# Kernel optimization log

Measured on AMD Instinct MI355X. Metric: run time of the kernel, lower is better.

Reference implementation:

```python
import jax, jax.numpy as jnp
import numpy as np
from jax import lax

EPS = 1e-5

def setup_inputs() -> dict:
    key = jax.random.key(0)
    k1, k2, k3, k4, k5 = jax.random.split(key, 5)
    N, Cin, L = 64, 64, 8192
    Cout, K = 128, 7
    return {
        "I": jax.random.normal(k1, (N, Cin, L), dtype=jnp.float32),
        "gamma": jax.random.uniform(k2, (Cin,), dtype=jnp.float32, minval=0.5, maxval=1.5),
        "beta": jax.random.normal(k3, (Cin,), dtype=jnp.float32) * 0.1,
        "W": jax.random.normal(k4, (Cout, Cin, K), dtype=jnp.float32) * 0.05,
        "alpha": jax.random.uniform(k5, (Cout, 1), dtype=jnp.float32, minval=0.01, maxval=0.2),
    }

def reference(I, gamma, beta, W, alpha):
    # BatchNorm1d (training mode: batch stats over N and L, biased variance)
    mean = jnp.mean(I, axis=(0, 2), keepdims=True)           # [1,C,1]
    var = jnp.mean(jnp.square(I - mean), axis=(0, 2), keepdims=True)
    x = (I - mean) * lax.rsqrt(var + EPS)
    x = x * gamma[None, :, None] + beta[None, :, None]
    # Binarize: sign with 0 -> +1
    xb = jnp.where(x >= 0, jnp.float32(1.0), jnp.float32(-1.0))
    # Conv1d (no bias), stride 1, pad 3; NCH x OIH -> NCH
    y = lax.conv_general_dilated(
        xb, W, window_strides=(1,), padding=[(3, 3)],
        dimension_numbers=("NCH", "OIH", "NCH"))
    # per-output-channel alpha scale: alpha [O,1] -> broadcast [1,O,1]
    y = y * alpha[None, :, :]
    # MaxPool1d(kernel=2, stride=2)
    y = lax.reduce_window(y, -jnp.inf, lax.max,
                          window_dimensions=(1, 1, 2),
                          window_strides=(1, 1, 2),
                          padding="VALID")
    return y  # [64, 128, 4096]
```

## Files before the change

### kernel.cpp

```cpp
#include <hip/hip_runtime.h>
#include <hip/hip_bf16.h>


#define N_S   64
#define C_IN  64
#define L_IN  8192
#define C_OUT 128
#define KW    7
#define L_OUT 4096
#define KDIM  448
#define XROWS 8200

typedef float  fx4   __attribute__((ext_vector_type(4)));
typedef short  s16x8 __attribute__((ext_vector_type(8)));

typedef __bf16 bfx8  __attribute__((ext_vector_type(8)));
template <typename V> struct OtherFrag          { typedef bfx8  type; };
template <>           struct OtherFrag<bfx8>    { typedef s16x8 type; };

template <typename V>
static __device__ inline auto mfma_sel(V a, V b, fx4 c, int)
    -> decltype(__builtin_amdgcn_mfma_f32_16x16x32_bf16(a, b, c, 0, 0, 0)) {
  return __builtin_amdgcn_mfma_f32_16x16x32_bf16(a, b, c, 0, 0, 0);
}
template <typename V>
static __device__ inline fx4 mfma_sel(V a, V b, fx4 c, long) {
  typedef typename OtherFrag<V>::type O;
  return __builtin_amdgcn_mfma_f32_16x16x32_bf16(
      __builtin_bit_cast(O, a), __builtin_bit_cast(O, b), c, 0, 0, 0);
}
static __device__ inline fx4 mfma_bf16(s16x8 a, s16x8 b, fx4 c) {
  return mfma_sel(a, b, c, 0);
}

static __device__ inline unsigned short bin_sign(float I, float m, float s,
                                                 float g, float b) {
  float x = __fadd_rn(__fmul_rn(__fmul_rn(__fsub_rn(I, m), s), g), b);
  return (x >= 0.0f) ? (unsigned short)0x3F80 : (unsigned short)0xBF80;
}

__global__ __launch_bounds__(256)
void bnstats_kernel(const float* __restrict__ x_in, double* __restrict__ partials) {
  const int c = blockIdx.x, g = blockIdx.y, tid = threadIdx.x;
  double sum = 0.0, sq = 0.0;
  for (int ns = 0; ns < 2; ++ns) {
    const float4* b4 =
        (const float4*)(x_in + ((size_t)((g * 2 + ns) * C_IN + c) << 13));
#pragma unroll
    for (int j = 0; j < 8; ++j) {
      float4 v = b4[j * 256 + tid];
      double dx = v.x, dy = v.y, dz = v.z, dw = v.w;
      sum += (dx + dy) + (dz + dw);
      sq  += (dx * dx + dy * dy) + (dz * dz + dw * dw);
    }
  }
  for (int off = 32; off > 0; off >>= 1) {
    sum += __shfl_down(sum, off);
    sq  += __shfl_down(sq,  off);
  }
  __shared__ double sd[8];
  const int wv = tid >> 6;
  if ((tid & 63) == 0) { sd[wv * 2] = sum; sd[wv * 2 + 1] = sq; }
  __syncthreads();
  if (tid == 0) {
    double S = sd[0] + sd[2] + sd[4] + sd[6];
    double Q = sd[1] + sd[3] + sd[5] + sd[7];
    partials[(c * 32 + g) * 2]     = S;
    partials[(c * 32 + g) * 2 + 1] = Q;
  }
}

__global__ void bnreduce_kernel(const double* __restrict__ partials,
                                const float* __restrict__ gamma,
                                const float* __restrict__ beta,
                                float4* __restrict__ bnparams) {
  const int c = threadIdx.x;
  if (c < C_IN) {
    double S = 0.0, Q = 0.0;
    for (int g = 0; g < 32; ++g) {
      S += partials[(c * 32 + g) * 2];
      Q += partials[(c * 32 + g) * 2 + 1];
    }
    const double NL = (double)N_S * (double)L_IN;
    double mean_d = S / NL;
    float  mean_f = (float)mean_d;
    double var_d = Q / NL - 2.0 * (double)mean_f * mean_d +
                   (double)mean_f * (double)mean_f;
    float var_f = (float)var_d;
    float vpe   = __fadd_rn(var_f, 1e-5f);
    float s_f   = (float)(1.0 / sqrt((double)vpe));
    bnparams[c] = make_float4(mean_f, s_f, gamma[c], beta[c]);
  }
}

__global__ __launch_bounds__(256)
void wrepack_kernel(const float* __restrict__ W, unsigned short* __restrict__ Wr) {
  const int f = blockIdx.x * 256 + threadIdx.x;
  if (f < C_OUT * KDIM) {
    const int o = f / KDIM, rem = f - o * KDIM;
    const int c = rem / KW, k = rem - c * KW;
    unsigned int u = __builtin_bit_cast(unsigned int, W[f]);
    u += 0x7FFFu + ((u >> 16) & 1u);
    Wr[o * KDIM + k * C_IN + c] = (unsigned short)(u >> 16);
  }
}

__global__ __launch_bounds__(256)
void bintrans2_kernel(const float* __restrict__ x_in,
                      const float4* __restrict__ bnparams,
                      unsigned short* __restrict__ xbt) {
  const int chunk = blockIdx.x, n = blockIdx.y, tid = threadIdx.x;
  const int lbase = chunk * 256;
  const int lane = tid & 63, w = tid >> 6;
  __shared__ __align__(16) char ldsT[256 * 128];

  const int fidx = (lbase >> 2) + lane;
#pragma unroll
  for (int cc = 0; cc < 4; ++cc) {
    const int c0 = w * 16 + cc * 4;
    const float4 bp0 = bnparams[c0 + 0];
    const float4 bp1 = bnparams[c0 + 1];
    const float4 bp2 = bnparams[c0 + 2];
    const float4 bp3 = bnparams[c0 + 3];
    const float4 f0 = ((const float4*)(x_in + ((size_t)(n * C_IN + c0 + 0) << 13)))[fidx];
    const float4 f1 = ((const float4*)(x_in + ((size_t)(n * C_IN + c0 + 1) << 13)))[fidx];
    const float4 f2 = ((const float4*)(x_in + ((size_t)(n * C_IN + c0 + 2) << 13)))[fidx];
    const float4 f3 = ((const float4*)(x_in + ((size_t)(n * C_IN + c0 + 3) << 13)))[fidx];
    const float e0[4] = {f0.x, f0.y, f0.z, f0.w};
    const float e1[4] = {f1.x, f1.y, f1.z, f1.w};
    const float e2[4] = {f2.x, f2.y, f2.z, f2.w};
    const float e3[4] = {f3.x, f3.y, f3.z, f3.w};
#pragma unroll
    for (int d = 0; d < 4; ++d) {
      ushort4 v;
      v.x = bin_sign(e0[d], bp0.x, bp0.y, bp0.z, bp0.w);
      v.y = bin_sign(e1[d], bp1.x, bp1.y, bp1.z, bp1.w);
      v.z = bin_sign(e2[d], bp2.x, bp2.y, bp2.z, bp2.w);
      v.w = bin_sign(e3[d], bp3.x, bp3.y, bp3.z, bp3.w);
      const int l   = 4 * lane + d;
      const int key = ((l & 7) ^ ((l >> 3) & 7)) << 4;
      *(ushort4*)(ldsT + l * 128 + ((c0 * 2) ^ key)) = v;
    }
  }
  __syncthreads();

  char* gout = (char*)xbt + (size_t)n * XROWS * 128 + (size_t)(lbase + 3) * 128;
#pragma unroll
  for (int i = 0; i < 8; ++i) {
    const int idx  = i * 256 + tid;
    const int row  = idx >> 3, slot = idx & 7;
    const int key  = ((row & 7) ^ ((row >> 3) & 7)) << 4;
    *(int4*)(gout + ((size_t)idx << 4)) =
        *(const int4*)(ldsT + row * 128 + ((slot << 4) ^ key));
  }
  int4 z4; z4.x = z4.y = z4.z = z4.w = 0;
  if (chunk == 0 && tid < 24)
    *(int4*)((char*)xbt + (size_t)n * XROWS * 128 + tid * 16) = z4;
  if (chunk == 31 && tid < 40)
    *(int4*)((char*)xbt + (size_t)n * XROWS * 128 + 8195ull * 128 + tid * 16) = z4;
}

__global__ __launch_bounds__(256)
void bconv3_kernel(const unsigned short* __restrict__ xbt,
                   const unsigned short* __restrict__ Wr,
                   const float* __restrict__ alpha,
                   float* __restrict__ out) {
  const int n     = blockIdx.z;
  const int obase = blockIdx.y * 64;
  const int lbase = blockIdx.x * 256;
  const int tid  = threadIdx.x;
  const int lane = tid & 63, w = tid >> 6;
  const int n16 = lane & 15, quad = lane >> 4;
  const int lW = w * 64;

  __shared__ __align__(16) char ldsB[264 * 128];

  {
    const char* gbase =
        (const char*)(xbt + (size_t)n * XROWS * C_IN) + (size_t)lbase * 128;
    const int r_in = lane >> 3;
    const int colb = (lane & 7) << 4;
    for (int i = w; i < 33; i += 4) {
      const int row = i * 8 + r_in;
      const char* src = gbase + row * 128 + (colb ^ ((row & 7) << 4));
      __builtin_amdgcn_global_load_lds((const unsigned int*)src,
                                       (unsigned int*)(ldsB + i * 1024),
                                       16, 0, 0);
    }
  }
  __syncthreads();

  fx4 acc[4][4];
#pragma unroll
  for (int ob = 0; ob < 4; ++ob)
#pragma unroll
    for (int lb = 0; lb < 4; ++lb)
      acc[ob][lb] = (fx4){0.f, 0.f, 0.f, 0.f};

  const unsigned short* arow = Wr + (obase + n16) * KDIM + quad * 8;

#pragma unroll
  for (int ks = 0; ks < 14; ++ks) {
    const int k  = ks >> 1;
    const int cb = ((ks & 1) << 6) | (quad << 4);
    s16x8 afr[4];
#pragma unroll
    for (int ob = 0; ob < 4; ++ob)
      afr[ob] = *(const s16x8*)(arow + ob * 16 * KDIM + ks * 32);
    s16x8 bfr[4];
#pragma unroll
    for (int lb = 0; lb < 4; ++lb) {
      const int row = lW + lb * 16 + n16 + k;
      bfr[lb] = *(const s16x8*)(ldsB + row * 128 + (cb ^ ((row & 7) << 4)));
    }
#pragma unroll
    for (int ob = 0; ob < 4; ++ob)
#pragma unroll
      for (int lb = 0; lb < 4; ++lb)
        acc[ob][lb] = mfma_bf16(afr[ob], bfr[lb], acc[ob][lb]);
  }

  float al[16];
#pragma unroll
  for (int ob = 0; ob < 4; ++ob)
#pragma unroll
    for (int r = 0; r < 4; ++r)
      al[ob * 4 + r] = alpha[obase + ob * 16 + quad * 4 + r];

  const size_t outbase = (size_t)n * C_OUT * L_OUT;
#pragma unroll
  for (int ob = 0; ob < 4; ++ob) {
#pragma unroll
    for (int lb = 0; lb < 4; ++lb) {
      const int l_local = lW + lb * 16 + n16;
#pragma unroll
      for (int r = 0; r < 4; ++r) {
        const int o = obase + ob * 16 + quad * 4 + r;
        float v  = acc[ob][lb][r];
        float pv = __shfl_xor(v, 1);
        float mx = fmaxf(v, pv);
        if ((n16 & 1) == 0) {
          out[outbase + (size_t)o * L_OUT + ((lbase + l_local) >> 1)] =
              mx * al[ob * 4 + r];
        }
      }
    }
  }
}

#define LT    64
#define PROWS 70
#define RS    72
__global__ __launch_bounds__(256)
void bconv_fused_kernel(const float* __restrict__ x_in,
                        const float4* __restrict__ bnparams,
                        const float* __restrict__ alpha,
                        const unsigned short* __restrict__ Wr,
                        float* __restrict__ out) {
  const int tile = blockIdx.x, n = blockIdx.y;
  const int l0 = tile * LT, tid = threadIdx.x;
  __shared__ __align__(16) unsigned short lds_xb[PROWS * RS];
  {
    const int c = tid >> 2, sub = tid & 3;
    const float4 bp = bnparams[c];
    const float* xc = x_in + ((size_t)(n * C_IN + c) << 13);
#pragma unroll
    for (int i = 0; i < 18; ++i) {
      const int p = sub * 18 + i;
      if (p < PROWS) {
        const int l = l0 + p - 3;
        unsigned short v = 0;
        if (l >= 0 && l < L_IN) v = bin_sign(xc[l], bp.x, bp.y, bp.z, bp.w);
        lds_xb[p * RS + c] = v;
      }
    }
  }
  __syncthreads();
  const int lane = tid & 63, w = tid >> 6;
  const int n16 = lane & 15, quad = lane >> 4;
  const int obase = (w & 1) * 64, lwave = (w >> 1) * 32;
  fx4 acc[4][2];
#pragma unroll
  for (int ob = 0; ob < 4; ++ob)
#pragma unroll
    for (int lb = 0; lb < 2; ++lb) acc[ob][lb] = (fx4){0.f, 0.f, 0.f, 0.f};
  const unsigned short* arow = Wr + (obase + n16) * KDIM + quad * 8;
#pragma unroll
  for (int ks = 0; ks < 14; ++ks) {
    const int k = ks >> 1, c0 = (ks & 1) * 32;
    s16x8 afr[4];
#pragma unroll
    for (int ob = 0; ob < 4; ++ob)
      afr[ob] = *(const s16x8*)(arow + ob * 16 * KDIM + ks * 32);
    s16x8 bfr[2];
#pragma unroll
    for (int lb = 0; lb < 2; ++lb) {
      const int p = lwave + lb * 16 + n16 + k;
      bfr[lb] = *(const s16x8*)(&lds_xb[p * RS + c0 + quad * 8]);
    }
#pragma unroll
    for (int ob = 0; ob < 4; ++ob)
#pragma unroll
      for (int lb = 0; lb < 2; ++lb)
        acc[ob][lb] = mfma_bf16(afr[ob], bfr[lb], acc[ob][lb]);
  }
  const size_t outbase = (size_t)n * C_OUT * L_OUT;
#pragma unroll
  for (int ob = 0; ob < 4; ++ob)
#pragma unroll
    for (int lb = 0; lb < 2; ++lb) {
      const int l_local = lwave + lb * 16 + n16;
#pragma unroll
      for (int r = 0; r < 4; ++r) {
        const int o = obase + ob * 16 + quad * 4 + r;
        float v = acc[ob][lb][r];
        float pv = __shfl_xor(v, 1);
        float mx = fmaxf(v, pv);
        if ((n16 & 1) == 0)
          out[outbase + (size_t)o * L_OUT + ((l0 + l_local) >> 1)] = mx * alpha[o];
      }
    }
}

extern "C" void kernel_launch(void* const* d_in, const int* in_sizes, int n_in,
                              void* d_out, int out_size, void* d_ws, size_t ws_size,
                              hipStream_t stream) {
  const float* x_in  = (const float*)d_in[0];
  const float* gamma = (const float*)d_in[1];
  const float* beta  = (const float*)d_in[2];
  const float* W     = (const float*)d_in[3];
  const float* alpha = (const float*)d_in[4];
  float* out = (float*)d_out;

  double*         partials = (double*)d_ws;
  float4*         bnparams = (float4*)((char*)d_ws + 32768);
  unsigned short* Wr       = (unsigned short*)((char*)d_ws + 36864);
  unsigned short* xbt      = (unsigned short*)((char*)d_ws + 262144);
  const size_t xbt_bytes   = (size_t)N_S * XROWS * C_IN * 2;

  bnstats_kernel<<<dim3(64, 32), 256, 0, stream>>>(x_in, partials);
  wrepack_kernel<<<(C_OUT * KDIM + 255) / 256, 256, 0, stream>>>(W, Wr);
  bnreduce_kernel<<<1, 64, 0, stream>>>(partials, gamma, beta, bnparams);

  if (ws_size >= 262144 + xbt_bytes) {
    bintrans2_kernel<<<dim3(32, 64), 256, 0, stream>>>(x_in, bnparams, xbt);
    bconv3_kernel<<<dim3(32, 2, 64), 256, 0, stream>>>(xbt, Wr, alpha, out);
  } else {
    bconv_fused_kernel<<<dim3(128, 64), 256, 0, stream>>>(x_in, bnparams,
                                                          alpha, Wr, out);
  }
}
```

Measured before the change: 423.5 us.

## Make bconv persistent with register-resident weights and double-buffered LDS staging

Replaces the one-tile-per-block conv with a kernel where each block loops over 16 L-tiles of 128. The full weight fragment set for 64 output channels stays in registers for the whole loop, and the next input tile is staged into LDS through a double buffer while the current one computes. Waves are split 2x2 over output channels and L. This cuts repeated weight loads from global memory and hides load latency. In exchange it uses a very large register footprint (occupancy bound of 1 block), and the grid shrinks to 256 blocks, which may underfill the GPU.

New measurement: 385.7 us. -8.9%, faster.

```diff
diff --git a/kernel.cpp b/kernel.cpp
--- a/kernel.cpp
+++ b/kernel.cpp
@@ -160,88 +160,107 @@
     *(int4*)((char*)xbt + (size_t)n * XROWS * 128 + 8195ull * 128 + tid * 16) = z4;
 }
 
-__global__ __launch_bounds__(256)
-void bconv3_kernel(const unsigned short* __restrict__ xbt,
+__global__ __launch_bounds__(256, 1)
+void bconv4_kernel(const unsigned short* __restrict__ xbt,
                    const unsigned short* __restrict__ Wr,
                    const float* __restrict__ alpha,
                    float* __restrict__ out) {
-  const int n     = blockIdx.z;
-  const int obase = blockIdx.y * 64;
-  const int lbase = blockIdx.x * 256;
+  const int n  = blockIdx.y;
+  const int lq = blockIdx.x;
   const int tid  = threadIdx.x;
   const int lane = tid & 63, w = tid >> 6;
   const int n16 = lane & 15, quad = lane >> 4;
-  const int lW = w * 64;
-
-  __shared__ __align__(16) char ldsB[264 * 128];
-
+  const int obase = (w & 1) * 64;
+  const int lW    = (w >> 1) * 64;
+
+  __shared__ __align__(16) char ldsB[2][136 * 128];
+
+  s16x8 areg[14][4];
   {
-    const char* gbase =
-        (const char*)(xbt + (size_t)n * XROWS * C_IN) + (size_t)lbase * 128;
-    const int r_in = lane >> 3;
-    const int colb = (lane & 7) << 4;
-    for (int i = w; i < 33; i += 4) {
+    const unsigned short* arow = Wr + (obase + n16) * KDIM + quad * 8;
+#pragma unroll
+    for (int ks = 0; ks < 14; ++ks)
+#pragma unroll
+      for (int ob = 0; ob < 4; ++ob)
+        areg[ks][ob] = *(const s16x8*)(arow + ob * 16 * KDIM + ks * 32);
+  }
+  float al[16];
+#pragma unroll
+  for (int ob = 0; ob < 4; ++ob)
+#pragma unroll
+    for (int r = 0; r < 4; ++r)
+      al[ob * 4 + r] = alpha[obase + ob * 16 + quad * 4 + r];
+
+  const char* gB = (const char*)(xbt + (size_t)n * XROWS * C_IN);
+  const int r_in = lane >> 3;
+  const int colb = (lane & 7) << 4;
+  const int lq0  = lq * 2048;
+
+  auto stage = [&](int t, int buf) {
+    const char* gbase = gB + (size_t)(lq0 + t * 128) * 128;
+    for (int i = w; i < 17; i += 4) {
       const int row = i * 8 + r_in;
       const char* src = gbase + row * 128 + (colb ^ ((row & 7) << 4));
       __builtin_amdgcn_global_load_lds((const unsigned int*)src,
-                                       (unsigned int*)(ldsB + i * 1024),
+                                       (unsigned int*)(&ldsB[buf][i * 1024]),
                                        16, 0, 0);
     }
-  }
+  };
+
+  stage(0, 0);
+  asm volatile("s_waitcnt vmcnt(0)");
   __syncthreads();
 
-  fx4 acc[4][4];
-#pragma unroll
-  for (int ob = 0; ob < 4; ++ob)
-#pragma unroll
-    for (int lb = 0; lb < 4; ++lb)
-      acc[ob][lb] = (fx4){0.f, 0.f, 0.f, 0.f};
-
-  const unsigned short* arow = Wr + (obase + n16) * KDIM + quad * 8;
-
-#pragma unroll
-  for (int ks = 0; ks < 14; ++ks) {
-    const int k  = ks >> 1;
-    const int cb = ((ks & 1) << 6) | (quad << 4);
-    s16x8 afr[4];
+  const size_t outbase = (size_t)n * C_OUT * L_OUT;
+  int buf = 0;
+  for (int t = 0; t < 16; ++t) {
+    if (t < 15) stage(t + 1, buf ^ 1);
+
+    fx4 acc[4][4];
 #pragma unroll
     for (int ob = 0; ob < 4; ++ob)
-      afr[ob] = *(const s16x8*)(arow + ob * 16 * KDIM + ks * 32);
-    s16x8 bfr[4];
-#pragma unroll
-    for (int lb = 0; lb < 4; ++lb) {
-      const int row = lW + lb * 16 + n16 + k;
-      bfr[lb] = *(const s16x8*)(ldsB + row * 128 + (cb ^ ((row & 7) << 4)));
-    }
-#pragma unroll
-    for (int ob = 0; ob < 4; ++ob)
 #pragma unroll
       for (int lb = 0; lb < 4; ++lb)
-        acc[ob][lb] = mfma_bf16(afr[ob], bfr[lb], acc[ob][lb]);
-  }
-
-  float al[16];
-#pragma unroll
-  for (int ob = 0; ob < 4; ++ob)
-#pragma unroll
-    for (int r = 0; r < 4; ++r)
-      al[ob * 4 + r] = alpha[obase + ob * 16 + quad * 4 + r];
-
-  const size_t outbase = (size_t)n * C_OUT * L_OUT;
-#pragma unroll
-  for (int ob = 0; ob < 4; ++ob) {
-#pragma unroll
-    for (int lb = 0; lb < 4; ++lb) {
-      const int l_local = lW + lb * 16 + n16;
-#pragma unroll
-      for (int r = 0; r < 4; ++r) {
-        const int o = obase + ob * 16 + quad * 4 + r;
-        float v  = acc[ob][lb][r];
-        float pv = __shfl_xor(v, 1);
-        float mx = fmaxf(v, pv);
-        if ((n16 & 1) == 0) {
-          out[outbase + (size_t)o * L_OUT + ((lbase + l_local) >> 1)] =
-              mx * al[ob * 4 + r];
+        acc[ob][lb] = (fx4){0.f, 0.f, 0.f, 0.f};
+
+    const char* Bb = ldsB[buf];
+#pragma unroll
+    for (int ks = 0; ks < 14; ++ks) {
+      const int k  = ks >> 1;
+      const int cb = ((ks & 1) << 6) | (quad << 4);
+      s16x8 bfr[4];
+#pragma unroll
+      for (int lb = 0; lb < 4; ++lb) {
+        const int row = lW + lb * 16 + n16 + k;
+        bfr[lb] = *(const s16x8*)(Bb + row * 128 + (cb ^ ((row & 7) << 4)));
+      }
+#pragma unroll
+      for (int ob = 0; ob < 4; ++ob)
+#pragma unroll
+        for (int lb = 0; lb < 4; ++lb)
+          acc[ob][lb] = mfma_bf16(areg[ks][ob], bfr[lb], acc[ob][lb]);
+    }
+
+    asm volatile("s_waitcnt vmcnt(0)");
+    __syncthreads();
+    buf ^= 1;
+
+    const int lstart = lq0 + t * 128;
+#pragma unroll
+    for (int ob = 0; ob < 4; ++ob) {
+#pragma unroll
+      for (int lb = 0; lb < 4; ++lb) {
+        const int l_local = lW + lb * 16 + n16;
+#pragma unroll
+        for (int r = 0; r < 4; ++r) {
+          const int o = obase + ob * 16 + quad * 4 + r;
+          float v  = acc[ob][lb][r];
+          float pv = __shfl_xor(v, 1);
+          float mx = fmaxf(v, pv);
+          if ((n16 & 1) == 0) {
+            out[outbase + (size_t)o * L_OUT + ((lstart + l_local) >> 1)] =
+                mx * al[ob * 4 + r];
+          }
         }
       }
     }
@@ -344,7 +363,7 @@
 
   if (ws_size >= 262144 + xbt_bytes) {
     bintrans2_kernel<<<dim3(32, 64), 256, 0, stream>>>(x_in, bnparams, xbt);
-    bconv3_kernel<<<dim3(32, 2, 64), 256, 0, stream>>>(xbt, Wr, alpha, out);
+    bconv4_kernel<<<dim3(4, 64), 256, 0, stream>>>(xbt, Wr, alpha, out);
   } else {
     bconv_fused_kernel<<<dim3(128, 64), 256, 0, stream>>>(x_in, bnparams,
                                                           alpha, Wr, out);
```
